# Performance work log

Hardware: AMD Instinct MI355X
Metric: run time of the kernel (lower is better)

## Reference

```python
import jax, jax.numpy as jnp
import numpy as np

B, N, D, E = 4, 16384, 128, 1048576  # batch, nodes/graph, hidden, total edges


def setup_inputs() -> dict:
    key = jax.random.key(0)
    k0, k1, k2, k3, k4, k5, k6 = jax.random.split(key, 7)
    x = jax.random.normal(k0, (B, N, D), dtype=jnp.float32)
    W = jax.random.normal(k1, (D, D), dtype=jnp.float32) * 0.05  # 'random_normal' init
    b = jax.random.normal(k2, (D,), dtype=jnp.float32) * 0.05
    edge_b = jax.random.randint(k3, (E,), 0, B, dtype=jnp.int32)
    edge_row = jax.random.randint(k4, (E,), 0, N, dtype=jnp.int32)
    edge_col = jax.random.randint(k5, (E,), 0, N, dtype=jnp.int32)
    edge_vals = jax.random.uniform(k6, (E,), dtype=jnp.float32)
    return {"x": x, "W": W, "b": b, "edge_b": edge_b, "edge_row": edge_row,
            "edge_col": edge_col, "edge_vals": edge_vals, "k": 2}


def reference(x, W, b, edge_b, edge_row, edge_col, edge_vals, k):
    # adj is a batched sparse [B, N, N]; edges stored as (batch, row, col, val) COO.
    seg_row = edge_b * N + edge_row  # flattened destination id in [0, B*N)
    # in_degrees = sum_j |adj[b, i, j]|
    deg = jax.ops.segment_sum(jnp.abs(edge_vals), seg_row, num_segments=B * N)
    deg = deg.reshape(B, N)
    norm = jnp.power(deg + 1e-6, -0.5)[..., None]          # [B, N, 1]
    norm_k = jnp.power(norm, k)                             # computed but unused (faithful to source)
    support = jnp.einsum('bnd,de->bne', x, W)               # x @ W
    y = (support * norm).reshape(B * N, D)                  # pre-normalized features
    # SpMM: out[b, i] = sum_{(b,i,j)} adj_val * y[b, j]
    msgs = y[edge_b * N + edge_col] * edge_vals[:, None]    # [E, D] gather + scale
    agg = jax.ops.segment_sum(msgs, seg_row, num_segments=B * N).reshape(B, N, D)
    return jax.nn.relu(agg * norm + b)
```

## Files before the change

### kernel.cpp

```cpp
#include <hip/hip_runtime.h>
#include <stdint.h>

#define B_ 4
#define N_ 16384
#define D_ 128
#define E_ 1048576
#define BN_ 65536
#define NBKT 256
#define NBLK 256
#define SCANB 64

typedef __attribute__((ext_vector_type(8))) short short8;
typedef __attribute__((ext_vector_type(4))) float floatx4;

static constexpr size_t OFF_Y      = 0;
static constexpr size_t OFF_PACK2  = 16777216;
static constexpr size_t OFF_HIST   = OFF_PACK2 + 8388608;
static constexpr size_t OFF_CURSOR = OFF_HIST + 262144;
static constexpr size_t OFF_NORM   = OFF_CURSOR + 262144;
static constexpr size_t OFF_BSUM   = OFF_NORM + 262144;
static constexpr size_t OFF_WH     = OFF_BSUM + 1024;
static constexpr size_t OFF_WL     = OFF_WH + 32768;

__device__ __forceinline__ uint32_t rne16(uint32_t u) {
    return (u + 0x7FFFu + ((u >> 16) & 1u)) >> 16;
}
__device__ __forceinline__ void bf16split(float f, uint16_t& h, uint16_t& l) {
    uint32_t hb = rne16(__float_as_uint(f));
    h = (uint16_t)hb;
    float r = f - __uint_as_float(hb << 16);
    l = (uint16_t)rne16(__float_as_uint(r));
}

__global__ __launch_bounds__(1024) void k_hist(const int* __restrict__ eb,
                                               const int* __restrict__ er,
                                               const float* __restrict__ Wg,
                                               uint32_t* __restrict__ histM,
                                               uint16_t* __restrict__ WhG,
                                               uint16_t* __restrict__ WlG) {
    __shared__ uint32_t h[NBKT];
    int t = threadIdx.x;
    if (t < NBKT) h[t] = 0;
    __syncthreads();
    if (blockIdx.x < 16) {
        int g = blockIdx.x * 1024 + t;
        float w = Wg[g];
        uint16_t hh, ll;
        bf16split(w, hh, ll);
        int k = g >> 7, n = g & 127;
        int o = ((k >> 3) * 128 + n) * 8 + (k & 7);
        WhG[o] = hh;
        WlG[o] = ll;
    }
    int vbase = blockIdx.x * 1024 + t;
    int4 b4 = ((const int4*)eb)[vbase];
    int4 r4 = ((const int4*)er)[vbase];
    atomicAdd(&h[(uint32_t)(b4.x * N_ + r4.x) >> 8], 1u);
    atomicAdd(&h[(uint32_t)(b4.y * N_ + r4.y) >> 8], 1u);
    atomicAdd(&h[(uint32_t)(b4.z * N_ + r4.z) >> 8], 1u);
    atomicAdd(&h[(uint32_t)(b4.w * N_ + r4.w) >> 8], 1u);
    __syncthreads();
    if (t < NBKT) histM[t * NBLK + blockIdx.x] = h[t];
}

__global__ __launch_bounds__(1024) void k_scan1(uint32_t* __restrict__ histM,
                                                uint32_t* __restrict__ bsum) {
    __shared__ uint32_t s[1024];
    int t = threadIdx.x;
    int g = blockIdx.x * 1024 + t;
    uint32_t v = histM[g];
    s[t] = v;
    __syncthreads();
    for (int off = 1; off < 1024; off <<= 1) {
        uint32_t a = (t >= off) ? s[t - off] : 0u;
        __syncthreads();
        s[t] += a;
        __syncthreads();
    }
    histM[g] = s[t] - v;
    if (t == 1023) bsum[blockIdx.x] = s[1023];
}

__global__ void k_scan2(uint32_t* bsum) {
    if (threadIdx.x == 0) {
        uint32_t acc = 0;
        for (int i = 0; i < SCANB; ++i) { uint32_t v = bsum[i]; bsum[i] = acc; acc += v; }
    }
}

__global__ __launch_bounds__(1024) void k_scatter(const int* __restrict__ eb,
                                                  const int* __restrict__ er,
                                                  const int* __restrict__ ec,
                                                  const float* __restrict__ ev,
                                                  const uint32_t* __restrict__ histM,
                                                  const uint32_t* __restrict__ bsum,
                                                  uint2* __restrict__ pack1) {
    __shared__ uint32_t cur[NBKT];
    int t = threadIdx.x;
    if (t < NBKT) cur[t] = histM[t * NBLK + blockIdx.x] + bsum[t >> 2];
    __syncthreads();
    int vbase = blockIdx.x * 1024 + t;
    int4   b4 = ((const int4*)eb)[vbase];
    int4   r4 = ((const int4*)er)[vbase];
    int4   c4 = ((const int4*)ec)[vbase];
    float4 v4 = ((const float4*)ev)[vbase];
    {
        uint32_t key = (uint32_t)(b4.x * N_ + r4.x);
        uint32_t pos = atomicAdd(&cur[key >> 8], 1u);
        pack1[pos] = make_uint2(((key & 255u) << 14) | (uint32_t)c4.x, __float_as_uint(v4.x));
    }
    {
        uint32_t key = (uint32_t)(b4.y * N_ + r4.y);
        uint32_t pos = atomicAdd(&cur[key >> 8], 1u);
        pack1[pos] = make_uint2(((key & 255u) << 14) | (uint32_t)c4.y, __float_as_uint(v4.y));
    }
    {
        uint32_t key = (uint32_t)(b4.z * N_ + r4.z);
        uint32_t pos = atomicAdd(&cur[key >> 8], 1u);
        pack1[pos] = make_uint2(((key & 255u) << 14) | (uint32_t)c4.z, __float_as_uint(v4.z));
    }
    {
        uint32_t key = (uint32_t)(b4.w * N_ + r4.w);
        uint32_t pos = atomicAdd(&cur[key >> 8], 1u);
        pack1[pos] = make_uint2(((key & 255u) << 14) | (uint32_t)c4.w, __float_as_uint(v4.w));
    }
}

__global__ __launch_bounds__(1024) void k_build(const uint32_t* __restrict__ histM,
                                                const uint32_t* __restrict__ bsum,
                                                const uint2* __restrict__ pack1,
                                                uint2* __restrict__ pack2,
                                                uint32_t* __restrict__ cursor,
                                                float* __restrict__ norm) {
    __shared__ uint32_t cnt[NBKT];
    __shared__ float    dsum[NBKT];
    __shared__ uint32_t scn[NBKT];
    __shared__ uint32_t rcur[NBKT];
    int t = threadIdx.x;
    int bkt = blockIdx.x;
    uint32_t bstart = histM[bkt * NBLK] + bsum[bkt >> 2];
    uint32_t bend = (bkt == NBKT - 1) ? E_
                    : histM[(bkt + 1) * NBLK] + bsum[(bkt + 1) >> 2];
    if (t < NBKT) { cnt[t] = 0; dsum[t] = 0.f; }
    __syncthreads();
    for (uint32_t i = bstart + t; i < bend; i += 1024) {
        uint2 p = pack1[i];
        uint32_t nl = p.x >> 14;
        atomicAdd(&cnt[nl], 1u);
        atomicAdd(&dsum[nl], fabsf(__uint_as_float(p.y)));
    }
    __syncthreads();
    if (t < NBKT) scn[t] = cnt[t];
    __syncthreads();
    for (int off = 1; off < NBKT; off <<= 1) {
        uint32_t a = 0;
        if (t < NBKT && t >= off) a = scn[t - off];
        __syncthreads();
        if (t < NBKT) scn[t] += a;
        __syncthreads();
    }
    if (t < NBKT) {
        uint32_t incl = scn[t];
        uint32_t excl = incl - cnt[t];
        rcur[t] = bstart + excl;
        cursor[bkt * NBKT + t] = bstart + incl;
        norm[bkt * NBKT + t] = rsqrtf(dsum[t] + 1e-6f);
    }
    __syncthreads();
    uint32_t colbase = (uint32_t)(bkt >> 6) * N_;
    for (uint32_t i = bstart + t; i < bend; i += 1024) {
        uint2 p = pack1[i];
        uint32_t nl = p.x >> 14;
        uint32_t pos = atomicAdd(&rcur[nl], 1u);
        pack2[pos] = make_uint2(colbase + (p.x & 0x3FFFu), p.y);
    }
}

__global__ __launch_bounds__(256) void k_matmul_mfma(const float* __restrict__ x,
                                                     const uint16_t* __restrict__ WhG,
                                                     const uint16_t* __restrict__ WlG,
                                                     const float* __restrict__ norm,
                                                     uint32_t* __restrict__ ybf) {
    __shared__ short WhS[16384];
    __shared__ short WlS[16384];
    __shared__ short XhS[4096];
    __shared__ short XlS[4096];
    __shared__ float normS[32];
    int tid = threadIdx.x;
    int row0 = blockIdx.x * 32;

    {
        const uint4* whg = (const uint4*)WhG;
        const uint4* wlg = (const uint4*)WlG;
        uint4* whs = (uint4*)WhS;
        uint4* wls = (uint4*)WlS;
#pragma unroll
        for (int i = 0; i < 8; ++i) {
            whs[i * 256 + tid] = whg[i * 256 + tid];
            wls[i * 256 + tid] = wlg[i * 256 + tid];
        }
    }
#pragma unroll
    for (int cc = 0; cc < 2; ++cc) {
        int c = cc * 256 + tid;
        int m = c & 31, kk = c >> 5;
        const float4* xp = (const float4*)(x + (size_t)(row0 + m) * D_ + kk * 8);
        float4 f0 = xp[0], f1 = xp[1];
        union { short8 v; uint16_t s[8]; } uh, ul;
        bf16split(f0.x, uh.s[0], ul.s[0]); bf16split(f0.y, uh.s[1], ul.s[1]);
        bf16split(f0.z, uh.s[2], ul.s[2]); bf16split(f0.w, uh.s[3], ul.s[3]);
        bf16split(f1.x, uh.s[4], ul.s[4]); bf16split(f1.y, uh.s[5], ul.s[5]);
        bf16split(f1.z, uh.s[6], ul.s[6]); bf16split(f1.w, uh.s[7], ul.s[7]);
        ((short8*)XhS)[c] = uh.v;
        ((short8*)XlS)[c] = ul.v;
    }
    if (tid < 32) normS[tid] = norm[row0 + tid];
    __syncthreads();

    int lane = tid & 63;
    int wv = tid >> 6;
    int quad = lane >> 4;
    int l15 = lane & 15;
    int wcol0 = wv * 32;
    floatx4 acc[2][2] = {};
    const short8* Xh8 = (const short8*)XhS;
    const short8* Xl8 = (const short8*)XlS;
    const short8* Wh8 = (const short8*)WhS;
    const short8* Wl8 = (const short8*)WlS;
#pragma unroll
    for (int ks = 0; ks < 4; ++ks) {
        int kkq = ks * 4 + quad;
        short8 ah0 = Xh8[kkq * 32 + l15];
        short8 ah1 = Xh8[kkq * 32 + 16 + l15];
        short8 al0 = Xl8[kkq * 32 + l15];
        short8 al1 = Xl8[kkq * 32 + 16 + l15];
        short8 bh0 = Wh8[kkq * 128 + wcol0 + l15];
        short8 bh1 = Wh8[kkq * 128 + wcol0 + 16 + l15];
        short8 bl0 = Wl8[kkq * 128 + wcol0 + l15];
        short8 bl1 = Wl8[kkq * 128 + wcol0 + 16 + l15];
        acc[0][0] = __builtin_amdgcn_mfma_f32_16x16x32_bf16(ah0, bh0, acc[0][0], 0, 0, 0);
        acc[0][1] = __builtin_amdgcn_mfma_f32_16x16x32_bf16(ah0, bh1, acc[0][1], 0, 0, 0);
        acc[1][0] = __builtin_amdgcn_mfma_f32_16x16x32_bf16(ah1, bh0, acc[1][0], 0, 0, 0);
        acc[1][1] = __builtin_amdgcn_mfma_f32_16x16x32_bf16(ah1, bh1, acc[1][1], 0, 0, 0);
        acc[0][0] = __builtin_amdgcn_mfma_f32_16x16x32_bf16(ah0, bl0, acc[0][0], 0, 0, 0);
        acc[0][1] = __builtin_amdgcn_mfma_f32_16x16x32_bf16(ah0, bl1, acc[0][1], 0, 0, 0);
        acc[1][0] = __builtin_amdgcn_mfma_f32_16x16x32_bf16(ah1, bl0, acc[1][0], 0, 0, 0);
        acc[1][1] = __builtin_amdgcn_mfma_f32_16x16x32_bf16(ah1, bl1, acc[1][1], 0, 0, 0);
        acc[0][0] = __builtin_amdgcn_mfma_f32_16x16x32_bf16(al0, bh0, acc[0][0], 0, 0, 0);
        acc[0][1] = __builtin_amdgcn_mfma_f32_16x16x32_bf16(al0, bh1, acc[0][1], 0, 0, 0);
        acc[1][0] = __builtin_amdgcn_mfma_f32_16x16x32_bf16(al1, bh0, acc[1][0], 0, 0, 0);
        acc[1][1] = __builtin_amdgcn_mfma_f32_16x16x32_bf16(al1, bh1, acc[1][1], 0, 0, 0);
    }

#pragma unroll
    for (int rt = 0; rt < 2; ++rt) {
#pragma unroll
        for (int ct = 0; ct < 2; ++ct) {
            floatx4 v = acc[rt][ct];
            int rbase = rt * 16 + quad * 4;
            int cp = (wcol0 + ct * 16) / 2 + (l15 >> 1);
#pragma unroll
            for (int r = 0; r < 4; ++r) {
                float mine = v[r] * normS[rbase + r];
                float oth = __shfl_xor(mine, 1, 64);
                uint32_t a = __float_as_uint((lane & 1) ? oth : mine);
                uint32_t b = __float_as_uint((lane & 1) ? mine : oth);
                uint32_t packed = rne16(a) | (rne16(b) << 16);
                bool doit = ((lane & 1) == 0) ? (r < 2) : (r >= 2);
                if (doit)
                    ybf[(size_t)(row0 + rbase + r) * 64 + cp] = packed;
            }
        }
    }
}

__device__ __forceinline__ void fma8(float* acc, float v, uint4 u) {
    acc[0] = fmaf(v, __uint_as_float(u.x << 16), acc[0]);
    acc[1] = fmaf(v, __uint_as_float(u.x & 0xFFFF0000u), acc[1]);
    acc[2] = fmaf(v, __uint_as_float(u.y << 16), acc[2]);
    acc[3] = fmaf(v, __uint_as_float(u.y & 0xFFFF0000u), acc[3]);
    acc[4] = fmaf(v, __uint_as_float(u.z << 16), acc[4]);
    acc[5] = fmaf(v, __uint_as_float(u.z & 0xFFFF0000u), acc[5]);
    acc[6] = fmaf(v, __uint_as_float(u.w << 16), acc[6]);
    acc[7] = fmaf(v, __uint_as_float(u.w & 0xFFFF0000u), acc[7]);
}

__global__ __launch_bounds__(256) void k_spmm(const uint32_t* __restrict__ cursor,
                                              const uint2* __restrict__ pack,
                                              const uint4* __restrict__ y4,
                                              const float* __restrict__ norm,
                                              const float* __restrict__ bias,
                                              float* __restrict__ out) {
    int node = blockIdx.x * 4 + (threadIdx.x >> 6);
    int lane = threadIdx.x & 63;
    int esub = lane >> 4;
    int chunk = lane & 15;
    uint32_t end = cursor[node];
    uint32_t start = (node == 0) ? 0u : cursor[node - 1];
    float acc[8] = {0.f,0.f,0.f,0.f,0.f,0.f,0.f,0.f};
    uint32_t e = start;
    for (; e + 16 <= end; e += 16) {
        uint2 pa = pack[e + 0 + esub];
        uint2 pb = pack[e + 4 + esub];
        uint2 pc = pack[e + 8 + esub];
        uint2 pd = pack[e + 12 + esub];
        uint4 ua = y4[(size_t)pa.x * 16 + chunk];
        uint4 ub = y4[(size_t)pb.x * 16 + chunk];
        uint4 uc = y4[(size_t)pc.x * 16 + chunk];
        uint4 ud = y4[(size_t)pd.x * 16 + chunk];
        fma8(acc, __uint_as_float(pa.y), ua);
        fma8(acc, __uint_as_float(pb.y), ub);
        fma8(acc, __uint_as_float(pc.y), uc);
        fma8(acc, __uint_as_float(pd.y), ud);
    }
    for (; e + 4 <= end; e += 4) {
        uint2 p = pack[e + esub];
        uint4 u = y4[(size_t)p.x * 16 + chunk];
        fma8(acc, __uint_as_float(p.y), u);
    }
    if (e < end) {
        uint32_t idx = e + esub;
        bool act = idx < end;
        uint2 p = pack[act ? idx : (end - 1)];
        uint4 u = y4[(size_t)p.x * 16 + chunk];
        float v = act ? __uint_as_float(p.y) : 0.f;
        fma8(acc, v, u);
    }
#pragma unroll
    for (int i = 0; i < 8; ++i) {
        acc[i] += __shfl_xor(acc[i], 16, 64);
        acc[i] += __shfl_xor(acc[i], 32, 64);
    }
    if (esub < 2) {
        float nm = norm[node];
        float4 bb = ((const float4*)bias)[chunk * 2 + esub];
        float4 o;
        o.x = fmaxf(fmaf(acc[esub * 4 + 0], nm, bb.x), 0.f);
        o.y = fmaxf(fmaf(acc[esub * 4 + 1], nm, bb.y), 0.f);
        o.z = fmaxf(fmaf(acc[esub * 4 + 2], nm, bb.z), 0.f);
        o.w = fmaxf(fmaf(acc[esub * 4 + 3], nm, bb.w), 0.f);
        ((float4*)out)[(size_t)node * 32 + chunk * 2 + esub] = o;
    }
}

extern "C" void kernel_launch(void* const* d_in, const int* in_sizes, int n_in,
                              void* d_out, int out_size, void* d_ws, size_t ws_size,
                              hipStream_t stream) {
    const float* x  = (const float*)d_in[0];
    const float* W  = (const float*)d_in[1];
    const float* bi = (const float*)d_in[2];
    const int* eb   = (const int*)d_in[3];
    const int* er   = (const int*)d_in[4];
    const int* ec   = (const int*)d_in[5];
    const float* ev = (const float*)d_in[6];
    float* out = (float*)d_out;

    char* ws = (char*)d_ws;
    uint32_t* ybf    = (uint32_t*)(ws + OFF_Y);
    uint2*    pack1  = (uint2*)(ws + OFF_Y);
    uint2*    pack2  = (uint2*)(ws + OFF_PACK2);
    uint32_t* histM  = (uint32_t*)(ws + OFF_HIST);
    uint32_t* cursor = (uint32_t*)(ws + OFF_CURSOR);
    float*    norm   = (float*)(ws + OFF_NORM);
    uint32_t* bsum   = (uint32_t*)(ws + OFF_BSUM);
    uint16_t* WhG    = (uint16_t*)(ws + OFF_WH);
    uint16_t* WlG    = (uint16_t*)(ws + OFF_WL);

    k_hist   <<<NBLK,  1024, 0, stream>>>(eb, er, W, histM, WhG, WlG);
    k_scan1  <<<SCANB, 1024, 0, stream>>>(histM, bsum);
    k_scan2  <<<1,     64,   0, stream>>>(bsum);
    k_scatter<<<NBLK,  1024, 0, stream>>>(eb, er, ec, ev, histM, bsum, pack1);
    k_build  <<<NBKT,  1024, 0, stream>>>(histM, bsum, pack1, pack2, cursor, norm);
    k_matmul_mfma<<<BN_ / 32, 256, 0, stream>>>(x, WhG, WlG, norm, ybf);
    k_spmm   <<<BN_ / 4, 256, 0, stream>>>(cursor, pack2, (const uint4*)ybf, norm, bi, out);
}
```

Baseline: 188.4 us.

## Replace histogram/scan bucketing with fixed-capacity buckets and global atomic cursors

Result: faster. 183.7 us (-2.4%).

```diff
diff --git a/kernel.cpp b/kernel.cpp
--- a/kernel.cpp
+++ b/kernel.cpp
@@ -8,18 +8,17 @@
 #define BN_ 65536
 #define NBKT 256
 #define NBLK 256
-#define SCANB 64
+#define CAP  6144
 
 typedef __attribute__((ext_vector_type(8))) short short8;
 typedef __attribute__((ext_vector_type(4))) float floatx4;
 
 static constexpr size_t OFF_Y      = 0;
 static constexpr size_t OFF_PACK2  = 16777216;
-static constexpr size_t OFF_HIST   = OFF_PACK2 + 8388608;
-static constexpr size_t OFF_CURSOR = OFF_HIST + 262144;
+static constexpr size_t OFF_GBKT   = OFF_PACK2 + 12582912;
+static constexpr size_t OFF_CURSOR = OFF_GBKT + 1024;
 static constexpr size_t OFF_NORM   = OFF_CURSOR + 262144;
-static constexpr size_t OFF_BSUM   = OFF_NORM + 262144;
-static constexpr size_t OFF_WH     = OFF_BSUM + 1024;
+static constexpr size_t OFF_WH     = OFF_NORM + 262144;
 static constexpr size_t OFF_WL     = OFF_WH + 32768;
 
 __device__ __forceinline__ uint32_t rne16(uint32_t u) {
@@ -32,16 +31,19 @@
     l = (uint16_t)rne16(__float_as_uint(r));
 }
 
-__global__ __launch_bounds__(1024) void k_hist(const int* __restrict__ eb,
-                                               const int* __restrict__ er,
-                                               const float* __restrict__ Wg,
-                                               uint32_t* __restrict__ histM,
-                                               uint16_t* __restrict__ WhG,
-                                               uint16_t* __restrict__ WlG) {
+__global__ __launch_bounds__(1024) void k_scatter(const int* __restrict__ eb,
+                                                  const int* __restrict__ er,
+                                                  const int* __restrict__ ec,
+                                                  const float* __restrict__ ev,
+                                                  const float* __restrict__ Wg,
+                                                  uint32_t* __restrict__ gbkt,
+                                                  uint2* __restrict__ pack1,
+                                                  uint16_t* __restrict__ WhG,
+                                                  uint16_t* __restrict__ WlG) {
+    __shared__ uint2    ed[4096];
     __shared__ uint32_t h[NBKT];
     int t = threadIdx.x;
     if (t < NBKT) h[t] = 0;
-    __syncthreads();
     if (blockIdx.x < 16) {
         int g = blockIdx.x * 1024 + t;
         float w = Wg[g];
@@ -52,82 +54,41 @@
         WhG[o] = hh;
         WlG[o] = ll;
     }
-    int vbase = blockIdx.x * 1024 + t;
-    int4 b4 = ((const int4*)eb)[vbase];
-    int4 r4 = ((const int4*)er)[vbase];
-    atomicAdd(&h[(uint32_t)(b4.x * N_ + r4.x) >> 8], 1u);
-    atomicAdd(&h[(uint32_t)(b4.y * N_ + r4.y) >> 8], 1u);
-    atomicAdd(&h[(uint32_t)(b4.z * N_ + r4.z) >> 8], 1u);
-    atomicAdd(&h[(uint32_t)(b4.w * N_ + r4.w) >> 8], 1u);
-    __syncthreads();
-    if (t < NBKT) histM[t * NBLK + blockIdx.x] = h[t];
-}
-
-__global__ __launch_bounds__(1024) void k_scan1(uint32_t* __restrict__ histM,
-                                                uint32_t* __restrict__ bsum) {
-    __shared__ uint32_t s[1024];
-    int t = threadIdx.x;
-    int g = blockIdx.x * 1024 + t;
-    uint32_t v = histM[g];
-    s[t] = v;
-    __syncthreads();
-    for (int off = 1; off < 1024; off <<= 1) {
-        uint32_t a = (t >= off) ? s[t - off] : 0u;
-        __syncthreads();
-        s[t] += a;
-        __syncthreads();
-    }
-    histM[g] = s[t] - v;
-    if (t == 1023) bsum[blockIdx.x] = s[1023];
-}
-
-__global__ void k_scan2(uint32_t* bsum) {
-    if (threadIdx.x == 0) {
-        uint32_t acc = 0;
-        for (int i = 0; i < SCANB; ++i) { uint32_t v = bsum[i]; bsum[i] = acc; acc += v; }
-    }
-}
-
-__global__ __launch_bounds__(1024) void k_scatter(const int* __restrict__ eb,
-                                                  const int* __restrict__ er,
-                                                  const int* __restrict__ ec,
-                                                  const float* __restrict__ ev,
-                                                  const uint32_t* __restrict__ histM,
-                                                  const uint32_t* __restrict__ bsum,
-                                                  uint2* __restrict__ pack1) {
-    __shared__ uint32_t cur[NBKT];
-    int t = threadIdx.x;
-    if (t < NBKT) cur[t] = histM[t * NBLK + blockIdx.x] + bsum[t >> 2];
     __syncthreads();
     int vbase = blockIdx.x * 1024 + t;
     int4   b4 = ((const int4*)eb)[vbase];
     int4   r4 = ((const int4*)er)[vbase];
     int4   c4 = ((const int4*)ec)[vbase];
     float4 v4 = ((const float4*)ev)[vbase];
-    {
-        uint32_t key = (uint32_t)(b4.x * N_ + r4.x);
-        uint32_t pos = atomicAdd(&cur[key >> 8], 1u);
-        pack1[pos] = make_uint2(((key & 255u) << 14) | (uint32_t)c4.x, __float_as_uint(v4.x));
-    }
-    {
-        uint32_t key = (uint32_t)(b4.y * N_ + r4.y);
-        uint32_t pos = atomicAdd(&cur[key >> 8], 1u);
-        pack1[pos] = make_uint2(((key & 255u) << 14) | (uint32_t)c4.y, __float_as_uint(v4.y));
-    }
-    {
-        uint32_t key = (uint32_t)(b4.z * N_ + r4.z);
-        uint32_t pos = atomicAdd(&cur[key >> 8], 1u);
-        pack1[pos] = make_uint2(((key & 255u) << 14) | (uint32_t)c4.z, __float_as_uint(v4.z));
-    }
-    {
-        uint32_t key = (uint32_t)(b4.w * N_ + r4.w);
-        uint32_t pos = atomicAdd(&cur[key >> 8], 1u);
-        pack1[pos] = make_uint2(((key & 255u) << 14) | (uint32_t)c4.w, __float_as_uint(v4.w));
-    }
-}
-
-__global__ __launch_bounds__(1024) void k_build(const uint32_t* __restrict__ histM,
-                                                const uint32_t* __restrict__ bsum,
+    uint32_t k0 = (uint32_t)(b4.x * N_ + r4.x);
+    uint32_t k1 = (uint32_t)(b4.y * N_ + r4.y);
+    uint32_t k2 = (uint32_t)(b4.z * N_ + r4.z);
+    uint32_t k3 = (uint32_t)(b4.w * N_ + r4.w);
+    ed[t * 4 + 0] = make_uint2((k0 << 14) | (uint32_t)c4.x, __float_as_uint(v4.x));
+    ed[t * 4 + 1] = make_uint2((k1 << 14) | (uint32_t)c4.y, __float_as_uint(v4.y));
+    ed[t * 4 + 2] = make_uint2((k2 << 14) | (uint32_t)c4.z, __float_as_uint(v4.z));
+    ed[t * 4 + 3] = make_uint2((k3 << 14) | (uint32_t)c4.w, __float_as_uint(v4.w));
+    atomicAdd(&h[k0 >> 8], 1u);
+    atomicAdd(&h[k1 >> 8], 1u);
+    atomicAdd(&h[k2 >> 8], 1u);
+    atomicAdd(&h[k3 >> 8], 1u);
+    __syncthreads();
+    if (t < NBKT) {
+        uint32_t c = h[t];
+        uint32_t base = c ? atomicAdd(&gbkt[t], c) : 0u;
+        h[t] = base;
+    }
+    __syncthreads();
+#pragma unroll
+    for (int i = 0; i < 4; ++i) {
+        uint2 en = ed[t * 4 + i];
+        uint32_t bkt = en.x >> 22;
+        uint32_t off = atomicAdd(&h[bkt], 1u);
+        pack1[(size_t)bkt * CAP + off] = make_uint2(en.x & 0x3FFFFFu, en.y);
+    }
+}
+
+__global__ __launch_bounds__(1024) void k_build(const uint32_t* __restrict__ gbkt,
                                                 const uint2* __restrict__ pack1,
                                                 uint2* __restrict__ pack2,
                                                 uint32_t* __restrict__ cursor,
@@ -138,9 +99,8 @@
     __shared__ uint32_t rcur[NBKT];
     int t = threadIdx.x;
     int bkt = blockIdx.x;
-    uint32_t bstart = histM[bkt * NBLK] + bsum[bkt >> 2];
-    uint32_t bend = (bkt == NBKT - 1) ? E_
-                    : histM[(bkt + 1) * NBLK] + bsum[(bkt + 1) >> 2];
+    uint32_t bstart = (uint32_t)bkt * CAP;
+    uint32_t bend = bstart + gbkt[bkt];
     if (t < NBKT) { cnt[t] = 0; dsum[t] = 0.f; }
     __syncthreads();
     for (uint32_t i = bstart + t; i < bend; i += 1024) {
@@ -291,12 +251,17 @@
                                               const float* __restrict__ norm,
                                               const float* __restrict__ bias,
                                               float* __restrict__ out) {
-    int node = blockIdx.x * 4 + (threadIdx.x >> 6);
+    int blk = blockIdx.x;
+    int xcd = blk & 7;
+    int j = blk >> 3;
+    int nodeblk = (xcd & 3) * 4096 + (xcd >> 2) * 2048 + j;
+    int node = nodeblk * 4 + (threadIdx.x >> 6);
     int lane = threadIdx.x & 63;
     int esub = lane >> 4;
     int chunk = lane & 15;
+    int nl = node & 255;
     uint32_t end = cursor[node];
-    uint32_t start = (node == 0) ? 0u : cursor[node - 1];
+    uint32_t start = (nl == 0) ? (uint32_t)(node >> 8) * CAP : cursor[node - 1];
     float acc[8] = {0.f,0.f,0.f,0.f,0.f,0.f,0.f,0.f};
     uint32_t e = start;
     for (; e + 16 <= end; e += 16) {
@@ -359,18 +324,15 @@
     uint32_t* ybf    = (uint32_t*)(ws + OFF_Y);
     uint2*    pack1  = (uint2*)(ws + OFF_Y);
     uint2*    pack2  = (uint2*)(ws + OFF_PACK2);
-    uint32_t* histM  = (uint32_t*)(ws + OFF_HIST);
+    uint32_t* gbkt   = (uint32_t*)(ws + OFF_GBKT);
     uint32_t* cursor = (uint32_t*)(ws + OFF_CURSOR);
     float*    norm   = (float*)(ws + OFF_NORM);
-    uint32_t* bsum   = (uint32_t*)(ws + OFF_BSUM);
     uint16_t* WhG    = (uint16_t*)(ws + OFF_WH);
     uint16_t* WlG    = (uint16_t*)(ws + OFF_WL);
 
-    k_hist   <<<NBLK,  1024, 0, stream>>>(eb, er, W, histM, WhG, WlG);
-    k_scan1  <<<SCANB, 1024, 0, stream>>>(histM, bsum);
-    k_scan2  <<<1,     64,   0, stream>>>(bsum);
-    k_scatter<<<NBLK,  1024, 0, stream>>>(eb, er, ec, ev, histM, bsum, pack1);
-    k_build  <<<NBKT,  1024, 0, stream>>>(histM, bsum, pack1, pack2, cursor, norm);
+    hipMemsetAsync(gbkt, 0, NBKT * sizeof(uint32_t), stream);
+    k_scatter<<<NBLK, 1024, 0, stream>>>(eb, er, ec, ev, W, gbkt, pack1, WhG, WlG);
+    k_build  <<<NBKT, 1024, 0, stream>>>(gbkt, pack1, pack2, cursor, norm);
     k_matmul_mfma<<<BN_ / 32, 256, 0, stream>>>(x, WhG, WlG, norm, ybf);
     k_spmm   <<<BN_ / 4, 256, 0, stream>>>(cursor, pack2, (const uint4*)ybf, norm, bi, out);
 }
```
